# Performance work log

Hardware: AMD Instinct MI355X
Metric: run time of the kernel (lower is better)

The kernel has to match this reference:

```python
import jax, jax.numpy as jnp
import numpy as np

D_MODEL = 256
N_HEADS = 8
N_LEVELS = 4
N_POINTS = 4
D_FFN = 1024
DH = D_MODEL // N_HEADS
SPATIAL = [(100, 100), (50, 50), (25, 25), (13, 13)]  # (H_l, W_l) per level


def setup_inputs() -> dict:
    key = jax.random.key(0)
    ks = iter(jax.random.split(key, 40))
    N, Lq = 8, 900
    Lin = sum(h * w for h, w in SPATIAL)
    p = lambda shape: jax.random.normal(next(ks), shape, jnp.float32) * 0.02
    inp = {
        'idx': 0,
        'tgt': jax.random.normal(next(ks), (N, Lq, D_MODEL), jnp.float32),
        'query_pos': jax.random.normal(next(ks), (N, Lq, D_MODEL), jnp.float32),
        'reference_points_def': jax.random.uniform(next(ks), (N, Lq, N_LEVELS, 2), jnp.float32),
        'src': jax.random.normal(next(ks), (N, Lin, D_MODEL), jnp.float32),
        'src_spatial_shapes': jnp.array(SPATIAL, jnp.int32),
        'level_start_index': jnp.array(np.cumsum([0] + [h * w for h, w in SPATIAL])[:-1], jnp.int32),
        'src_padding_mask': jnp.zeros((N, Lin), bool),
        # self-attn params
        'wq': p((D_MODEL, D_MODEL)), 'bq': jnp.zeros((D_MODEL,)),
        'wk': p((D_MODEL, D_MODEL)), 'bk': jnp.zeros((D_MODEL,)),
        'wv': p((D_MODEL, D_MODEL)), 'bv': jnp.zeros((D_MODEL,)),
        'wo': p((D_MODEL, D_MODEL)), 'bo': jnp.zeros((D_MODEL,)),
        # MSDeformAttn params
        'w_val': p((D_MODEL, D_MODEL)), 'b_val': jnp.zeros((D_MODEL,)),
        'w_off': p((D_MODEL, N_HEADS * N_LEVELS * N_POINTS * 2)), 'b_off': p((N_HEADS * N_LEVELS * N_POINTS * 2,)),
        'w_att': p((D_MODEL, N_HEADS * N_LEVELS * N_POINTS)), 'b_att': jnp.zeros((N_HEADS * N_LEVELS * N_POINTS,)),
        'w_out': p((D_MODEL, D_MODEL)), 'b_out': jnp.zeros((D_MODEL,)),
        # layer norms
        'ln1_g': jnp.ones((D_MODEL,)), 'ln1_b': jnp.zeros((D_MODEL,)),
        'ln2_g': jnp.ones((D_MODEL,)), 'ln2_b': jnp.zeros((D_MODEL,)),
        'ln3_g': jnp.ones((D_MODEL,)), 'ln3_b': jnp.zeros((D_MODEL,)),
        # FFN
        'w1': p((D_MODEL, D_FFN)), 'b1': jnp.zeros((D_FFN,)),
        'w2': p((D_FFN, D_MODEL)), 'b2': jnp.zeros((D_MODEL,)),
    }
    return inp


def _ln(x, g, b):
    m = x.mean(-1, keepdims=True)
    v = jnp.var(x, axis=-1, keepdims=True)
    return (x - m) / jnp.sqrt(v + 1e-5) * g + b


def _mha(q, k, v, wq, bq, wk, bk, wv, bv, wo, bo):
    N, Lq, _ = q.shape
    split = lambda x: x.reshape(N, -1, N_HEADS, DH).transpose(0, 2, 1, 3)  # (N,H,L,dh)
    qh = split(q @ wq + bq) * (1.0 / np.sqrt(DH))
    kh = split(k @ wk + bk)
    vh = split(v @ wv + bv)
    attn = jax.nn.softmax(jnp.einsum('bhqd,bhkd->bhqk', qh, kh), axis=-1)
    o = jnp.einsum('bhqk,bhkd->bhqd', attn, vh).transpose(0, 2, 1, 3).reshape(N, Lq, D_MODEL)
    return o @ wo + bo


def _bilinear(vflat, Hl, Wl, loc):
    # vflat: (N, H, Hl*Wl, dh); loc: (N, Lq, H, P, 2) normalized (x, y) in [0,1]
    N, Lq, _, P, _ = loc.shape
    x = loc[..., 0] * Wl - 0.5  # align_corners=False pixel coords
    y = loc[..., 1] * Hl - 0.5
    x0 = jnp.floor(x); y0 = jnp.floor(y)
    fx = (x - x0).transpose(0, 2, 1, 3).reshape(N, N_HEADS, Lq * P, 1)
    fy = (y - y0).transpose(0, 2, 1, 3).reshape(N, N_HEADS, Lq * P, 1)
    x0i = x0.astype(jnp.int32); y0i = y0.astype(jnp.int32)

    def gather(xi, yi):
        valid = ((xi >= 0) & (xi < Wl) & (yi >= 0) & (yi < Hl)).astype(vflat.dtype)
        idx = jnp.clip(yi, 0, Hl - 1) * Wl + jnp.clip(xi, 0, Wl - 1)
        idx = idx.transpose(0, 2, 1, 3).reshape(N, N_HEADS, Lq * P)
        g = jnp.take_along_axis(vflat, idx[..., None], axis=2)  # (N,H,Lq*P,dh)
        return g * valid.transpose(0, 2, 1, 3).reshape(N, N_HEADS, Lq * P, 1)

    v = (gather(x0i, y0i) * (1 - fx) * (1 - fy)
         + gather(x0i + 1, y0i) * fx * (1 - fy)
         + gather(x0i, y0i + 1) * (1 - fx) * fy
         + gather(x0i + 1, y0i + 1) * fx * fy)
    return v.reshape(N, N_HEADS, Lq, P, DH)


def _msdeform(query, ref, src, ss, pad_mask, w_val, b_val, w_off, b_off, w_att, b_att, w_out, b_out):
    N, Lq, _ = query.shape
    value = src @ w_val + b_val
    value = jnp.where(pad_mask[..., None], 0.0, value)  # masked_fill on padded memory
    off = (query @ w_off + b_off).reshape(N, Lq, N_HEADS, N_LEVELS, N_POINTS, 2)
    att = jax.nn.softmax((query @ w_att + b_att).reshape(N, Lq, N_HEADS, N_LEVELS * N_POINTS), axis=-1)
    att = att.reshape(N, Lq, N_HEADS, N_LEVELS, N_POINTS)
    normalizer = jnp.array([[w, h] for h, w in ss], jnp.float32)  # (L, 2) as (W_l, H_l)
    loc = ref[:, :, None, :, None, :] + off / normalizer[None, None, None, :, None, :]
    out = jnp.zeros((N, N_HEADS, Lq, DH), value.dtype)
    start = 0
    for l, (Hl, Wl) in enumerate(ss):
        vflat = value[:, start:start + Hl * Wl].reshape(N, Hl * Wl, N_HEADS, DH).transpose(0, 2, 1, 3)
        samp = _bilinear(vflat, Hl, Wl, loc[:, :, :, l])  # (N,H,Lq,P,dh)
        w_l = att[:, :, :, l].transpose(0, 2, 1, 3)  # (N,H,Lq,P)
        out = out + (samp * w_l[..., None]).sum(3)
        start += Hl * Wl
    out = out.transpose(0, 2, 1, 3).reshape(N, Lq, D_MODEL)
    return out @ w_out + b_out, loc


def reference(idx, tgt, query_pos, reference_points_def, src, src_spatial_shapes, level_start_index,
              src_padding_mask, wq, bq, wk, bk, wv, bv, wo, bo,
              w_val, b_val, w_off, b_off, w_att, b_att, w_out, b_out,
              ln1_g, ln1_b, ln2_g, ln2_b, ln3_g, ln3_b, w1, b1, w2, b2):
    ss = [tuple(int(v) for v in row) for row in np.asarray(src_spatial_shapes)]
    # self-attention (is_contrastive=False path)
    q = tgt + query_pos
    tgt2 = _mha(q, q, tgt, wq, bq, wk, bk, wv, bv, wo, bo)
    tgt = _ln(tgt + tgt2, ln2_g, ln2_b)
    # multiscale deformable cross-attention
    tgt2, _ = _msdeform(tgt + query_pos, reference_points_def, src, ss, src_padding_mask,
                        w_val, b_val, w_off, b_off, w_att, b_att, w_out, b_out)
    tgt = _ln(tgt + tgt2, ln1_g, ln1_b)
    # FFN
    tgt2 = jax.nn.relu(tgt @ w1 + b1) @ w2 + b2
    tgt = _ln(tgt + tgt2, ln3_g, ln3_b)
    return tgt
```

## Files before the change

### kernel.cpp

```cpp
#include <hip/hip_runtime.h>
#include <math.h>

#define NB 8
#define LQ 900
#define DM 256
#define NH 8
#define DH 32
#define NL 4
#define NP 4
#define DFFN 1024
#define LIN 13294
#define NVAL (NB*LIN)
#define MROW (NB*LQ)

typedef __attribute__((ext_vector_type(8))) short bf16x8;
typedef __attribute__((ext_vector_type(4))) float f32x4;

__device__ __forceinline__ unsigned short f2bf(float x) {
  unsigned u = __float_as_uint(x);
  u += 0x7FFFu + ((u >> 16) & 1u);
  return (unsigned short)(u >> 16);
}

__global__ __launch_bounds__(256) void add_kernel(const float* __restrict__ a,
                                                  const float* __restrict__ b,
                                                  float* __restrict__ c, int n4) {
  int i = blockIdx.x * 256 + threadIdx.x;
  if (i < n4) {
    float4 x = ((const float4*)a)[i];
    float4 y = ((const float4*)b)[i];
    ((float4*)c)[i] = make_float4(x.x + y.x, x.y + y.y, x.z + y.z, x.w + y.w);
  }
}

__global__ __launch_bounds__(256) void pack_w(const float* __restrict__ Win,
                                              unsigned short* __restrict__ Wp) {
  const int idx = blockIdx.x * 256 + threadIdx.x;
  const int e = idx & 7;
  const int cs = (idx >> 3) & 3;
  const int n = (idx >> 5) & 255;
  const int kt = idx >> 13;
  const int c = cs ^ ((n >> 1) & 3);
  const int k = kt * 32 + c * 8 + e;
  Wp[idx] = f2bf(Win[(size_t)k * 256 + n]);
}

__global__ __launch_bounds__(256) void value_gemm2(const float* __restrict__ A,
                                                   const unsigned short* __restrict__ Wp,
                                                   const float* __restrict__ bias,
                                                   unsigned short* __restrict__ C,
                                                   int M) {
  __shared__ char lds[17408];
  short* As = (short*)lds;
  short* Bs = (short*)(lds + 4096);
  const int tid = threadIdx.x;
  const int lane = tid & 63, w = tid >> 6;
  const int wr = w >> 1, wc = w & 1;
  const int l15 = lane & 15, lc = lane >> 4;
  const int nwg = gridDim.x;
  const int qq = nwg >> 3, rr = nwg & 7;
  const int xcd = blockIdx.x & 7, pos = blockIdx.x >> 3;
  const int wgid = (xcd < rr ? xcd * (qq + 1) : rr * (qq + 1) + (xcd - rr) * qq) + pos;
  const int m0 = (wgid >> 1) * 64, n0 = (wgid & 1) * 128;
  const int ar = tid >> 2, ac = tid & 3;
  f32x4 acc[2][4] = {};
  for (int kt = 0; kt < 8; kt++) {
    const int arow = min(m0 + ar, M - 1);
    const float* ap = A + (size_t)arow * 256 + kt * 32 + ac * 8;
    const float4 a0 = ((const float4*)ap)[0], a1 = ((const float4*)ap)[1];
    const unsigned short* bp = Wp + ((size_t)(kt * 256 + n0)) * 32 + tid * 16;
    const uint4 b0 = ((const uint4*)bp)[0], b1 = ((const uint4*)bp)[1];
    __syncthreads();
    {
      bf16x8 av;
      av[0] = (short)f2bf(a0.x); av[1] = (short)f2bf(a0.y);
      av[2] = (short)f2bf(a0.z); av[3] = (short)f2bf(a0.w);
      av[4] = (short)f2bf(a1.x); av[5] = (short)f2bf(a1.y);
      av[6] = (short)f2bf(a1.z); av[7] = (short)f2bf(a1.w);
      *(bf16x8*)&As[ar * 32 + ((ac ^ ((ar >> 1) & 3)) << 3)] = av;
      *(uint4*)&Bs[tid * 16] = b0;
      *(uint4*)&Bs[tid * 16 + 8] = b1;
    }
    __syncthreads();
    bf16x8 af[2], bq[4];
#pragma unroll
    for (int i = 0; i < 2; i++) {
      const int row = wr * 32 + i * 16 + l15;
      af[i] = *(const bf16x8*)&As[row * 32 + ((lc ^ ((row >> 1) & 3)) << 3)];
    }
#pragma unroll
    for (int q = 0; q < 4; q++) {
      const int col = wc * 64 + q * 16 + l15;
      bq[q] = *(const bf16x8*)&Bs[col * 32 + ((lc ^ ((col >> 1) & 3)) << 3)];
    }
#pragma unroll
    for (int i = 0; i < 2; i++)
#pragma unroll
      for (int q = 0; q < 4; q++)
        acc[i][q] = __builtin_amdgcn_mfma_f32_16x16x32_bf16(af[i], bq[q], acc[i][q], 0, 0, 0);
  }
  __syncthreads();
  short* strip = (short*)lds + w * 2176;
  float bv[4];
#pragma unroll
  for (int q = 0; q < 4; q++) bv[q] = bias[n0 + wc * 64 + q * 16 + l15];
#pragma unroll
  for (int i = 0; i < 2; i++)
#pragma unroll
    for (int q = 0; q < 4; q++)
#pragma unroll
      for (int r = 0; r < 4; r++)
        strip[(i * 16 + lc * 4 + r) * 68 + q * 16 + l15] = (short)f2bf(acc[i][q][r] + bv[q]);
  __syncthreads();
#pragma unroll
  for (int p = 0; p < 4; p++) {
    const int row = p * 8 + (lane >> 3), c8 = lane & 7;
    const bf16x8 v = *(const bf16x8*)&strip[row * 68 + c8 * 8];
    const int grow = m0 + wr * 32 + row;
    if (grow < M)
      *(bf16x8*)(C + (size_t)grow * 256 + n0 + wc * 64 + c8 * 8) = v;
  }
}

#define LDSW 40
__global__ __launch_bounds__(256) void gemm_bf16(const float* __restrict__ A,
                                                 const float* __restrict__ W,
                                                 const float* __restrict__ bias,
                                                 float* __restrict__ C,
                                                 int M, int Nn, int K, float scale, int relu,
                                                 int out_bf16) {
  __shared__ short As[64 * LDSW];
  __shared__ short Bs[64 * LDSW];
  const int tid = threadIdx.x;
  const int lane = tid & 63, w = tid >> 6;
  const int wr = w >> 1, wc = w & 1;
  const int m0 = blockIdx.y << 6, n0 = blockIdx.x << 6;
  const int ar = tid >> 2, ac = (tid & 3) << 3;
  const int bk = tid >> 3, bn = (tid & 7) << 3;
  const int aswz = (((ac >> 3) ^ (ar >> 3)) & 3) << 3;
  const int l15 = lane & 15, lc = lane >> 4;
  f32x4 acc[2][2] = {};
  for (int kt = 0; kt < K; kt += 32) {
    float4 a0 = make_float4(0.f, 0.f, 0.f, 0.f), a1 = a0;
    if (m0 + ar < M) {
      const float* ap = A + (size_t)(m0 + ar) * K + kt + ac;
      a0 = ((const float4*)ap)[0]; a1 = ((const float4*)ap)[1];
    }
    const float* wp = W + (size_t)(kt + bk) * Nn + n0 + bn;
    const float4 b0 = ((const float4*)wp)[0], b1 = ((const float4*)wp)[1];
    __syncthreads();
    {
      bf16x8 av;
      av[0] = (short)f2bf(a0.x); av[1] = (short)f2bf(a0.y);
      av[2] = (short)f2bf(a0.z); av[3] = (short)f2bf(a0.w);
      av[4] = (short)f2bf(a1.x); av[5] = (short)f2bf(a1.y);
      av[6] = (short)f2bf(a1.z); av[7] = (short)f2bf(a1.w);
      *(bf16x8*)&As[ar * LDSW + aswz] = av;
      unsigned short bb[8] = {f2bf(b0.x), f2bf(b0.y), f2bf(b0.z), f2bf(b0.w),
                              f2bf(b1.x), f2bf(b1.y), f2bf(b1.z), f2bf(b1.w)};
      const int bchunk = bk >> 3, bke = bk & 7;
#pragma unroll
      for (int j = 0; j < 8; j++) {
        const int n = bn + j;
        Bs[n * LDSW + (((bchunk ^ (n >> 3)) & 3) << 3) + bke] = (short)bb[j];
      }
    }
    __syncthreads();
    bf16x8 af[2], bf[2];
#pragma unroll
    for (int i = 0; i < 2; i++) {
      const int row = wr * 32 + i * 16 + l15;
      af[i] = *(const bf16x8*)&As[row * LDSW + (((lc ^ (row >> 3)) & 3) << 3)];
      const int col = wc * 32 + i * 16 + l15;
      bf[i] = *(const bf16x8*)&Bs[col * LDSW + (((lc ^ (col >> 3)) & 3) << 3)];
    }
#pragma unroll
    for (int i = 0; i < 2; i++)
#pragma unroll
      for (int j = 0; j < 2; j++)
        acc[i][j] = __builtin_amdgcn_mfma_f32_16x16x32_bf16(af[i], bf[j], acc[i][j], 0, 0, 0);
  }
#pragma unroll
  for (int i = 0; i < 2; i++) {
    const int row0 = m0 + wr * 32 + i * 16 + lc * 4;
#pragma unroll
    for (int j = 0; j < 2; j++) {
      const int col = n0 + wc * 32 + j * 16 + l15;
      const float bv = bias[col];
#pragma unroll
      for (int r = 0; r < 4; r++) {
        const int row = row0 + r;
        if (row < M) {
          float v = (acc[i][j][r] + bv) * scale;
          if (relu) v = fmaxf(v, 0.f);
          if (out_bf16)
            ((unsigned short*)C)[(size_t)row * Nn + col] = f2bf(v);
          else
            C[(size_t)row * Nn + col] = v;
        }
      }
    }
  }
}

__global__ __launch_bounds__(256) void attn_mfma(const float* __restrict__ Qg,
                                                 const float* __restrict__ Kg,
                                                 const float* __restrict__ Vg,
                                                 float* __restrict__ O) {
  __shared__ short Ks[2048];
  __shared__ short Vt[2048];
  __shared__ short Pl[4096];
  const int tid = threadIdx.x;
  const int lane = tid & 63, w = tid >> 6;
  const int l15 = lane & 15, lc = lane >> 4;
  const int h = blockIdx.y, b = blockIdx.z;
  const int q0 = blockIdx.x * 64;
  char* KsB = (char*)Ks; char* VtB = (char*)Vt; char* PlB = (char*)Pl + w * 2048;

  bf16x8 qa;
  {
    const int qrow = min(q0 + w * 16 + l15, LQ - 1);
    const float* qp = Qg + ((size_t)(b * LQ + qrow)) * DM + h * DH + lc * 8;
    const float4 qx = ((const float4*)qp)[0], qy = ((const float4*)qp)[1];
    qa[0] = (short)f2bf(qx.x); qa[1] = (short)f2bf(qx.y);
    qa[2] = (short)f2bf(qx.z); qa[3] = (short)f2bf(qx.w);
    qa[4] = (short)f2bf(qy.x); qa[5] = (short)f2bf(qy.y);
    qa[6] = (short)f2bf(qy.z); qa[7] = (short)f2bf(qy.w);
  }
  f32x4 o0 = {0.f, 0.f, 0.f, 0.f}, o1 = {0.f, 0.f, 0.f, 0.f};
  float mrow[4], lrow[4];
#pragma unroll
  for (int r = 0; r < 4; r++) { mrow[r] = -1e30f; lrow[r] = 0.f; }
  const int skey = tid >> 2, sq = tid & 3;

  for (int kt = 0; kt < LQ; kt += 64) {
    const int kr = min(kt + skey, LQ - 1);
    const float* kp = Kg + ((size_t)(b * LQ + kr)) * DM + h * DH + sq * 8;
    const float* vp = Vg + ((size_t)(b * LQ + kr)) * DM + h * DH + sq * 8;
    const float4 k0 = ((const float4*)kp)[0], k1 = ((const float4*)kp)[1];
    const float4 v0 = ((const float4*)vp)[0], v1 = ((const float4*)vp)[1];
    __syncthreads();
    {
      bf16x8 kb;
      kb[0] = (short)f2bf(k0.x); kb[1] = (short)f2bf(k0.y);
      kb[2] = (short)f2bf(k0.z); kb[3] = (short)f2bf(k0.w);
      kb[4] = (short)f2bf(k1.x); kb[5] = (short)f2bf(k1.y);
      kb[6] = (short)f2bf(k1.z); kb[7] = (short)f2bf(k1.w);
      *(bf16x8*)(KsB + ((skey * 64 + sq * 16) ^ ((skey & 7) << 4))) = kb;
      unsigned short vv[8] = {f2bf(v0.x), f2bf(v0.y), f2bf(v0.z), f2bf(v0.w),
                              f2bf(v1.x), f2bf(v1.y), f2bf(v1.z), f2bf(v1.w)};
#pragma unroll
      for (int j = 0; j < 8; j++) {
        const int dh = sq * 8 + j;
        const int qz = ((dh & 7) ^ (((dh >> 3) & 3) << 1)) << 4;
        *(short*)(VtB + ((dh * 128 + skey * 2) ^ qz)) = (short)vv[j];
      }
    }
    __syncthreads();
    f32x4 s[4];
#pragma unroll
    for (int cb = 0; cb < 4; cb++) {
      const int key = cb * 16 + l15;
      const bf16x8 kf = *(const bf16x8*)(KsB + ((key * 64 + lc * 16) ^ ((key & 7) << 4)));
      const f32x4 z = {0.f, 0.f, 0.f, 0.f};
      s[cb] = __builtin_amdgcn_mfma_f32_16x16x32_bf16(qa, kf, z, 0, 0, 0);
    }
#pragma unroll
    for (int cb = 0; cb < 4; cb++)
      if (kt + cb * 16 + l15 >= LQ) {
        s[cb][0] = -1e30f; s[cb][1] = -1e30f; s[cb][2] = -1e30f; s[cb][3] = -1e30f;
      }
    float tm[4], fs[4], ps[4];
#pragma unroll
    for (int r = 0; r < 4; r++)
      tm[r] = fmaxf(fmaxf(s[0][r], s[1][r]), fmaxf(s[2][r], s[3][r]));
#pragma unroll
    for (int msk = 1; msk <= 8; msk <<= 1)
#pragma unroll
      for (int r = 0; r < 4; r++) tm[r] = fmaxf(tm[r], __shfl_xor(tm[r], msk));
#pragma unroll
    for (int r = 0; r < 4; r++) {
      const float nm = fmaxf(mrow[r], tm[r]);
      fs[r] = __expf(mrow[r] - nm);
      mrow[r] = nm;
    }
#pragma unroll
    for (int cb = 0; cb < 4; cb++)
#pragma unroll
      for (int r = 0; r < 4; r++) s[cb][r] = __expf(s[cb][r] - mrow[r]);
#pragma unroll
    for (int r = 0; r < 4; r++) ps[r] = (s[0][r] + s[1][r]) + (s[2][r] + s[3][r]);
#pragma unroll
    for (int msk = 1; msk <= 8; msk <<= 1)
#pragma unroll
      for (int r = 0; r < 4; r++) ps[r] += __shfl_xor(ps[r], msk);
#pragma unroll
    for (int r = 0; r < 4; r++) {
      lrow[r] = lrow[r] * fs[r] + ps[r];
      o0[r] *= fs[r]; o1[r] *= fs[r];
    }
#pragma unroll
    for (int cb = 0; cb < 4; cb++)
#pragma unroll
      for (int r = 0; r < 4; r++) {
        const int row = lc * 4 + r, col = cb * 16 + l15;
        *(short*)(PlB + ((row * 128 + col * 2) ^ ((row & 7) << 4))) = (short)f2bf(s[cb][r]);
      }
#pragma unroll
    for (int ks2 = 0; ks2 < 2; ks2++) {
      const int koff2 = (ks2 * 32 + lc * 8) * 2;
      const bf16x8 pa = *(const bf16x8*)(PlB + ((l15 * 128 + koff2) ^ ((l15 & 7) << 4)));
      {
        const int dh = l15;
        const int qz = ((dh & 7) ^ (((dh >> 3) & 3) << 1)) << 4;
        const bf16x8 vf = *(const bf16x8*)(VtB + ((dh * 128 + koff2) ^ qz));
        o0 = __builtin_amdgcn_mfma_f32_16x16x32_bf16(pa, vf, o0, 0, 0, 0);
      }
      {
        const int dh = 16 + l15;
        const int qz = ((dh & 7) ^ (((dh >> 3) & 3) << 1)) << 4;
        const bf16x8 vf = *(const bf16x8*)(VtB + ((dh * 128 + koff2) ^ qz));
        o1 = __builtin_amdgcn_mfma_f32_16x16x32_bf16(pa, vf, o1, 0, 0, 0);
      }
    }
  }
#pragma unroll
  for (int r = 0; r < 4; r++) {
    const int qrow = q0 + w * 16 + lc * 4 + r;
    if (qrow < LQ) {
      const float inv = 1.f / lrow[r];
      float* op = O + ((size_t)(b * LQ + qrow)) * DM + h * DH;
      op[l15] = o0[r] * inv;
      op[16 + l15] = o1[r] * inv;
    }
  }
}

__global__ __launch_bounds__(256) void sample_kernel(const unsigned short* __restrict__ value,
                                                     const float* __restrict__ ref,
                                                     const float* __restrict__ off,
                                                     const float* __restrict__ att,
                                                     float* __restrict__ out) {
  const int t = blockIdx.x * 256 + threadIdx.x;
  const int d8 = t & 3;
  const int h = (t >> 2) & 7;
  const int qb = t >> 5;
  const int b = qb / LQ;
  const int HLs[4] = {100, 50, 25, 13};
  const int STs[4] = {0, 10000, 12500, 13125};
  const float* rp = ref + (size_t)qb * (NL * 2);
  const float* op = off + (size_t)qb * DM + h * (NL * NP * 2);
  const float* ap = att + (size_t)qb * (NH * NL * NP) + h * (NL * NP);
  const unsigned short* vb = value + (size_t)b * LIN * DM + h * DH + d8 * 8;

  float aw[16];
#pragma unroll
  for (int i = 0; i < 4; i++) {
    const float4 a4 = ((const float4*)ap)[i];
    aw[4 * i] = a4.x; aw[4 * i + 1] = a4.y; aw[4 * i + 2] = a4.z; aw[4 * i + 3] = a4.w;
  }
  float am = aw[0];
#pragma unroll
  for (int i = 1; i < 16; i++) am = fmaxf(am, aw[i]);
  float asum = 0.f;
#pragma unroll
  for (int i = 0; i < 16; i++) { aw[i] = __expf(aw[i] - am); asum += aw[i]; }
  const float ainv = 1.f / asum;

  float acc[8] = {};
#pragma unroll
  for (int l = 0; l < NL; l++) {
    const int Hl = HLs[l], Wl = HLs[l], st = STs[l];
    const float rx = rp[l * 2], ry = rp[l * 2 + 1];
#pragma unroll
    for (int p = 0; p < NP; p++) {
      const float2 o2 = ((const float2*)op)[l * NP + p];
      const float a = aw[l * NP + p] * ainv;
      const float locx = rx + o2.x / (float)Wl;
      const float locy = ry + o2.y / (float)Hl;
      const float x = locx * (float)Wl - 0.5f;
      const float y = locy * (float)Hl - 0.5f;
      const float xf = floorf(x), yf = floorf(y);
      const float fx = x - xf, fy = y - yf;
      const int x0 = (int)xf, y0 = (int)yf;
      const int x1 = x0 + 1, y1 = y0 + 1;
      const float vx0 = (x0 >= 0 && x0 < Wl) ? 1.f : 0.f;
      const float vx1 = (x1 >= 0 && x1 < Wl) ? 1.f : 0.f;
      const float vy0 = (y0 >= 0 && y0 < Hl) ? 1.f : 0.f;
      const float vy1 = (y1 >= 0 && y1 < Hl) ? 1.f : 0.f;
      const int cx0 = min(max(x0, 0), Wl - 1), cx1 = min(max(x1, 0), Wl - 1);
      const int cy0 = min(max(y0, 0), Hl - 1), cy1 = min(max(y1, 0), Hl - 1);
      const float w00 = a * (1.f - fx) * (1.f - fy) * vx0 * vy0;
      const float w10 = a * fx * (1.f - fy) * vx1 * vy0;
      const float w01 = a * (1.f - fx) * fy * vx0 * vy1;
      const float w11 = a * fx * fy * vx1 * vy1;
      const unsigned short* r0 = vb + (size_t)(st + cy0 * Wl) * DM;
      const unsigned short* r1 = vb + (size_t)(st + cy1 * Wl) * DM;
      const uint4 g00 = *(const uint4*)(r0 + (size_t)cx0 * DM);
      const uint4 g10 = *(const uint4*)(r0 + (size_t)cx1 * DM);
      const uint4 g01 = *(const uint4*)(r1 + (size_t)cx0 * DM);
      const uint4 g11 = *(const uint4*)(r1 + (size_t)cx1 * DM);
      const unsigned u00[4] = {g00.x, g00.y, g00.z, g00.w};
      const unsigned u10[4] = {g10.x, g10.y, g10.z, g10.w};
      const unsigned u01[4] = {g01.x, g01.y, g01.z, g01.w};
      const unsigned u11[4] = {g11.x, g11.y, g11.z, g11.w};
#pragma unroll
      for (int i = 0; i < 4; i++) {
        acc[2 * i]     += w00 * __uint_as_float(u00[i] << 16) + w10 * __uint_as_float(u10[i] << 16)
                        + w01 * __uint_as_float(u01[i] << 16) + w11 * __uint_as_float(u11[i] << 16);
        acc[2 * i + 1] += w00 * __uint_as_float(u00[i] & 0xFFFF0000u) + w10 * __uint_as_float(u10[i] & 0xFFFF0000u)
                        + w01 * __uint_as_float(u01[i] & 0xFFFF0000u) + w11 * __uint_as_float(u11[i] & 0xFFFF0000u);
      }
    }
  }
  float* o = out + (size_t)t * 8;
  *(float4*)o = make_float4(acc[0], acc[1], acc[2], acc[3]);
  *(float4*)(o + 4) = make_float4(acc[4], acc[5], acc[6], acc[7]);
}

__global__ __launch_bounds__(64) void ln_kernel(const float* __restrict__ A,
                                                const float* __restrict__ R,
                                                const float* __restrict__ g,
                                                const float* __restrict__ be,
                                                float* __restrict__ out) {
  const int row = blockIdx.x, t = threadIdx.x;
  const float4 va = ((const float4*)(A + (size_t)row * DM))[t];
  const float4 vr = ((const float4*)(R + (size_t)row * DM))[t];
  const float x0 = va.x + vr.x, x1 = va.y + vr.y, x2 = va.z + vr.z, x3 = va.w + vr.w;
  float s = x0 + x1 + x2 + x3;
  float ss = x0 * x0 + x1 * x1 + x2 * x2 + x3 * x3;
#pragma unroll
  for (int o = 1; o < 64; o <<= 1) { s += __shfl_xor(s, o); ss += __shfl_xor(ss, o); }
  const float mean = s * (1.f / DM);
  const float var = ss * (1.f / DM) - mean * mean;
  const float rstd = rsqrtf(var + 1e-5f);
  const float4 vg = ((const float4*)g)[t];
  const float4 vb = ((const float4*)be)[t];
  float4 o4;
  o4.x = (x0 - mean) * rstd * vg.x + vb.x;
  o4.y = (x1 - mean) * rstd * vg.y + vb.y;
  o4.z = (x2 - mean) * rstd * vg.z + vb.z;
  o4.w = (x3 - mean) * rstd * vg.w + vb.w;
  ((float4*)(out + (size_t)row * DM))[t] = o4;
}

extern "C" void kernel_launch(void* const* d_in, const int* in_sizes, int n_in,
                              void* d_out, int out_size, void* d_ws, size_t ws_size,
                              hipStream_t stream) {
  const float* tgt  = (const float*)d_in[1];
  const float* qpos = (const float*)d_in[2];
  const float* ref  = (const float*)d_in[3];
  const float* src  = (const float*)d_in[4];
  const float* wq = (const float*)d_in[8];  const float* bq = (const float*)d_in[9];
  const float* wk = (const float*)d_in[10]; const float* bk = (const float*)d_in[11];
  const float* wv = (const float*)d_in[12]; const float* bv = (const float*)d_in[13];
  const float* wo = (const float*)d_in[14]; const float* bo = (const float*)d_in[15];
  const float* w_val = (const float*)d_in[16]; const float* b_val = (const float*)d_in[17];
  const float* w_off = (const float*)d_in[18]; const float* b_off = (const float*)d_in[19];
  const float* w_att = (const float*)d_in[20]; const float* b_att = (const float*)d_in[21];
  const float* w_out = (const float*)d_in[22]; const float* b_out = (const float*)d_in[23];
  const float* ln1g = (const float*)d_in[24]; const float* ln1b = (const float*)d_in[25];
  const float* ln2g = (const float*)d_in[26]; const float* ln2b = (const float*)d_in[27];
  const float* ln3g = (const float*)d_in[28]; const float* ln3b = (const float*)d_in[29];
  const float* w1 = (const float*)d_in[30]; const float* b1 = (const float*)d_in[31];
  const float* w2 = (const float*)d_in[32]; const float* b2 = (const float*)d_in[33];

  const size_t S = (size_t)MROW * DM;
  const size_t VAL_F = (size_t)NVAL * DM;
  float* ws = (float*)d_ws;
  float* value = ws;
  unsigned short* wp = (unsigned short*)(ws + VAL_F / 2);
  float* B0   = ws + VAL_F;
  float* qin  = B0 + 0 * S;
  float* Qb   = B0 + 1 * S;
  float* Kb   = B0 + 2 * S;
  float* Vb   = B0 + 3 * S;
  float* Ob   = B0 + 4 * S;
  float* tmp  = B0 + 5 * S;
  float* x1   = B0 + 0 * S;
  float* q2   = B0 + 1 * S;
  float* offb = B0 + 2 * S;
  float* attb = B0 + 3 * S;
  float* samp = B0 + 4 * S;
  float* x2   = B0 + 6 * S;
  float* hffn = B0 + 1 * S;

  const float qscale = 0.17677669529663687f;
  const int n4 = (int)(S / 4);
  const dim3 blk(256);
  const dim3 gAdd((n4 + 255) / 256);
  const dim3 gQ(DM / 64, (MROW + 63) / 64);
  const dim3 gAtt(2, (MROW + 63) / 64);
  const dim3 gF1(DFFN / 64, (MROW + 63) / 64);
  const int gVal2 = 2 * ((NVAL + 63) / 64);

  add_kernel<<<gAdd, blk, 0, stream>>>(tgt, qpos, qin, n4);
  gemm_bf16<<<gQ, blk, 0, stream>>>(qin, wq, bq, Qb, MROW, DM, DM, qscale, 0, 0);
  gemm_bf16<<<gQ, blk, 0, stream>>>(qin, wk, bk, Kb, MROW, DM, DM, 1.f, 0, 0);
  gemm_bf16<<<gQ, blk, 0, stream>>>(tgt, wv, bv, Vb, MROW, DM, DM, 1.f, 0, 0);
  attn_mfma<<<dim3((LQ + 63) / 64, NH, NB), blk, 0, stream>>>(Qb, Kb, Vb, Ob);
  gemm_bf16<<<gQ, blk, 0, stream>>>(Ob, wo, bo, tmp, MROW, DM, DM, 1.f, 0, 0);
  ln_kernel<<<dim3(MROW), dim3(64), 0, stream>>>(tmp, tgt, ln2g, ln2b, x1);

  pack_w<<<dim3(256), blk, 0, stream>>>(w_val, wp);
  value_gemm2<<<dim3(gVal2), blk, 0, stream>>>(src, wp, b_val, (unsigned short*)value, NVAL);
  add_kernel<<<gAdd, blk, 0, stream>>>(x1, qpos, q2, n4);
  gemm_bf16<<<gQ, blk, 0, stream>>>(q2, w_off, b_off, offb, MROW, DM, DM, 1.f, 0, 0);
  gemm_bf16<<<gAtt, blk, 0, stream>>>(q2, w_att, b_att, attb, MROW, NH * NL * NP, DM, 1.f, 0, 0);
  sample_kernel<<<dim3((MROW * NH * 4) / 256), blk, 0, stream>>>(
      (const unsigned short*)value, ref, offb, attb, samp);
  gemm_bf16<<<gQ, blk, 0, stream>>>(samp, w_out, b_out, tmp, MROW, DM, DM, 1.f, 0, 0);
  ln_kernel<<<dim3(MROW), dim3(64), 0, stream>>>(tmp, x1, ln1g, ln1b, x2);

  gemm_bf16<<<gF1, blk, 0, stream>>>(x2, w1, b1, hffn, MROW, DFFN, DM, 1.f, 1, 0);
  gemm_bf16<<<gQ, blk, 0, stream>>>(hffn, w2, b2, tmp, MROW, DM, DFFN, 1.f, 0, 0);
  ln_kernel<<<dim3(MROW), dim3(64), 0, stream>>>(tmp, x2, ln3g, ln3b, (float*)d_out);
}
```

Before: 279.7 us.

## Fuse residual adds into GEMMs, batch QKV and offset/attn GEMMs, use bf16 intermediates

Removes the two elementwise add kernels by folding the query_pos add into the A-operand load of the GEMMs. The Q/K/V projections become one launch indexed by blockIdx.z, and so do the offset and attention-weight projections. Q/K/V and the FFN hidden activations are now stored as bf16, which halves intermediate traffic and drops the conversions in attention and the second FFN GEMM. The cost is extra branching in a shared GEMM body, and out-of-range A rows are now clamped instead of zero-filled.

```diff
diff --git a/kernel.cpp b/kernel.cpp
--- a/kernel.cpp
+++ b/kernel.cpp
@@ -20,17 +20,6 @@
   unsigned u = __float_as_uint(x);
   u += 0x7FFFu + ((u >> 16) & 1u);
   return (unsigned short)(u >> 16);
-}
-
-__global__ __launch_bounds__(256) void add_kernel(const float* __restrict__ a,
-                                                  const float* __restrict__ b,
-                                                  float* __restrict__ c, int n4) {
-  int i = blockIdx.x * 256 + threadIdx.x;
-  if (i < n4) {
-    float4 x = ((const float4*)a)[i];
-    float4 y = ((const float4*)b)[i];
-    ((float4*)c)[i] = make_float4(x.x + y.x, x.y + y.y, x.z + y.z, x.w + y.w);
-  }
 }
 
 __global__ __launch_bounds__(256) void pack_w(const float* __restrict__ Win,
@@ -123,38 +112,43 @@
 }
 
 #define LDSW 40
-__global__ __launch_bounds__(256) void gemm_bf16(const float* __restrict__ A,
-                                                 const float* __restrict__ W,
-                                                 const float* __restrict__ bias,
-                                                 float* __restrict__ C,
-                                                 int M, int Nn, int K, float scale, int relu,
-                                                 int out_bf16) {
-  __shared__ short As[64 * LDSW];
-  __shared__ short Bs[64 * LDSW];
+__device__ __forceinline__ void gemm_body(const void* Aptr, const float* A2,
+                                          const float* __restrict__ W,
+                                          const float* __restrict__ bias, void* Cptr,
+                                          int M, int Nn, int K, float scale, int relu,
+                                          int a_bf16, int out_bf16, int m0, int n0,
+                                          short* As, short* Bs) {
   const int tid = threadIdx.x;
   const int lane = tid & 63, w = tid >> 6;
   const int wr = w >> 1, wc = w & 1;
-  const int m0 = blockIdx.y << 6, n0 = blockIdx.x << 6;
   const int ar = tid >> 2, ac = (tid & 3) << 3;
   const int bk = tid >> 3, bn = (tid & 7) << 3;
   const int aswz = (((ac >> 3) ^ (ar >> 3)) & 3) << 3;
   const int l15 = lane & 15, lc = lane >> 4;
+  const int arow = min(m0 + ar, M - 1);
   f32x4 acc[2][2] = {};
   for (int kt = 0; kt < K; kt += 32) {
-    float4 a0 = make_float4(0.f, 0.f, 0.f, 0.f), a1 = a0;
-    if (m0 + ar < M) {
-      const float* ap = A + (size_t)(m0 + ar) * K + kt + ac;
-      a0 = ((const float4*)ap)[0]; a1 = ((const float4*)ap)[1];
+    bf16x8 av;
+    if (a_bf16) {
+      av = *(const bf16x8*)((const unsigned short*)Aptr + (size_t)arow * K + kt + ac);
+    } else {
+      const float* ap = (const float*)Aptr + (size_t)arow * K + kt + ac;
+      float4 a0 = ((const float4*)ap)[0], a1 = ((const float4*)ap)[1];
+      if (A2) {
+        const float* a2p = A2 + (size_t)arow * K + kt + ac;
+        const float4 c0 = ((const float4*)a2p)[0], c1 = ((const float4*)a2p)[1];
+        a0.x += c0.x; a0.y += c0.y; a0.z += c0.z; a0.w += c0.w;
+        a1.x += c1.x; a1.y += c1.y; a1.z += c1.z; a1.w += c1.w;
+      }
+      av[0] = (short)f2bf(a0.x); av[1] = (short)f2bf(a0.y);
+      av[2] = (short)f2bf(a0.z); av[3] = (short)f2bf(a0.w);
+      av[4] = (short)f2bf(a1.x); av[5] = (short)f2bf(a1.y);
+      av[6] = (short)f2bf(a1.z); av[7] = (short)f2bf(a1.w);
     }
     const float* wp = W + (size_t)(kt + bk) * Nn + n0 + bn;
     const float4 b0 = ((const float4*)wp)[0], b1 = ((const float4*)wp)[1];
     __syncthreads();
     {
-      bf16x8 av;
-      av[0] = (short)f2bf(a0.x); av[1] = (short)f2bf(a0.y);
-      av[2] = (short)f2bf(a0.z); av[3] = (short)f2bf(a0.w);
-      av[4] = (short)f2bf(a1.x); av[5] = (short)f2bf(a1.y);
-      av[6] = (short)f2bf(a1.z); av[7] = (short)f2bf(a1.w);
       *(bf16x8*)&As[ar * LDSW + aswz] = av;
       unsigned short bb[8] = {f2bf(b0.x), f2bf(b0.y), f2bf(b0.z), f2bf(b0.w),
                               f2bf(b1.x), f2bf(b1.y), f2bf(b1.z), f2bf(b1.w)};
@@ -194,18 +188,62 @@
           float v = (acc[i][j][r] + bv) * scale;
           if (relu) v = fmaxf(v, 0.f);
           if (out_bf16)
-            ((unsigned short*)C)[(size_t)row * Nn + col] = f2bf(v);
+            ((unsigned short*)Cptr)[(size_t)row * Nn + col] = f2bf(v);
           else
-            C[(size_t)row * Nn + col] = v;
+            ((float*)Cptr)[(size_t)row * Nn + col] = v;
         }
       }
     }
   }
 }
 
-__global__ __launch_bounds__(256) void attn_mfma(const float* __restrict__ Qg,
-                                                 const float* __restrict__ Kg,
-                                                 const float* __restrict__ Vg,
+__global__ __launch_bounds__(256) void gemm_qkv(const float* __restrict__ tgt,
+                                                const float* __restrict__ qpos,
+                                                const float* __restrict__ wq, const float* __restrict__ bq_,
+                                                const float* __restrict__ wk, const float* __restrict__ bk_,
+                                                const float* __restrict__ wv, const float* __restrict__ bv_,
+                                                unsigned short* Qb, unsigned short* Kb, unsigned short* Vb,
+                                                float qscale) {
+  __shared__ short As[64 * LDSW];
+  __shared__ short Bs[64 * LDSW];
+  const int z = blockIdx.z;
+  const float* W = (z == 0) ? wq : (z == 1) ? wk : wv;
+  const float* bias = (z == 0) ? bq_ : (z == 1) ? bk_ : bv_;
+  unsigned short* C = (z == 0) ? Qb : (z == 1) ? Kb : Vb;
+  const float* A2 = (z == 2) ? nullptr : qpos;
+  gemm_body(tgt, A2, W, bias, C, MROW, DM, DM, (z == 0) ? qscale : 1.f, 0, 0, 1,
+            blockIdx.y * 64, blockIdx.x * 64, As, Bs);
+}
+
+__global__ __launch_bounds__(256) void gemm_offatt(const float* __restrict__ x1,
+                                                   const float* __restrict__ qpos,
+                                                   const float* __restrict__ w_off, const float* __restrict__ b_off,
+                                                   const float* __restrict__ w_att, const float* __restrict__ b_att,
+                                                   float* offb, float* attb) {
+  const int z = blockIdx.z;
+  if (z == 1 && blockIdx.x >= 2) return;
+  __shared__ short As[64 * LDSW];
+  __shared__ short Bs[64 * LDSW];
+  const float* W = z ? w_att : w_off;
+  const float* bias = z ? b_att : b_off;
+  float* C = z ? attb : offb;
+  const int Nn = z ? 128 : 256;
+  gemm_body(x1, qpos, W, bias, C, MROW, Nn, DM, 1.f, 0, 0, 0,
+            blockIdx.y * 64, blockIdx.x * 64, As, Bs);
+}
+
+__global__ __launch_bounds__(256) void gemm_fused(const void* A, const float* W, const float* bias,
+                                                  void* C, int M, int Nn, int K, float scale,
+                                                  int relu, int a_bf16, int out_bf16) {
+  __shared__ short As[64 * LDSW];
+  __shared__ short Bs[64 * LDSW];
+  gemm_body(A, nullptr, W, bias, C, M, Nn, K, scale, relu, a_bf16, out_bf16,
+            blockIdx.y * 64, blockIdx.x * 64, As, Bs);
+}
+
+__global__ __launch_bounds__(256) void attn_mfma(const unsigned short* __restrict__ Qg,
+                                                 const unsigned short* __restrict__ Kg,
+                                                 const unsigned short* __restrict__ Vg,
                                                  float* __restrict__ O) {
   __shared__ short Ks[2048];
   __shared__ short Vt[2048];
@@ -220,12 +258,7 @@
   bf16x8 qa;
   {
     const int qrow = min(q0 + w * 16 + l15, LQ - 1);
-    const float* qp = Qg + ((size_t)(b * LQ + qrow)) * DM + h * DH + lc * 8;
-    const float4 qx = ((const float4*)qp)[0], qy = ((const float4*)qp)[1];
-    qa[0] = (short)f2bf(qx.x); qa[1] = (short)f2bf(qx.y);
-    qa[2] = (short)f2bf(qx.z); qa[3] = (short)f2bf(qx.w);
-    qa[4] = (short)f2bf(qy.x); qa[5] = (short)f2bf(qy.y);
-    qa[6] = (short)f2bf(qy.z); qa[7] = (short)f2bf(qy.w);
+    qa = *(const bf16x8*)(Qg + ((size_t)(b * LQ + qrow)) * DM + h * DH + lc * 8);
   }
   f32x4 o0 = {0.f, 0.f, 0.f, 0.f}, o1 = {0.f, 0.f, 0.f, 0.f};
   float mrow[4], lrow[4];
@@ -235,20 +268,11 @@
 
   for (int kt = 0; kt < LQ; kt += 64) {
     const int kr = min(kt + skey, LQ - 1);
-    const float* kp = Kg + ((size_t)(b * LQ + kr)) * DM + h * DH + sq * 8;
-    const float* vp = Vg + ((size_t)(b * LQ + kr)) * DM + h * DH + sq * 8;
-    const float4 k0 = ((const float4*)kp)[0], k1 = ((const float4*)kp)[1];
-    const float4 v0 = ((const float4*)vp)[0], v1 = ((const float4*)vp)[1];
+    const bf16x8 kb = *(const bf16x8*)(Kg + ((size_t)(b * LQ + kr)) * DM + h * DH + sq * 8);
+    const bf16x8 vv = *(const bf16x8*)(Vg + ((size_t)(b * LQ + kr)) * DM + h * DH + sq * 8);
     __syncthreads();
     {
-      bf16x8 kb;
-      kb[0] = (short)f2bf(k0.x); kb[1] = (short)f2bf(k0.y);
-      kb[2] = (short)f2bf(k0.z); kb[3] = (short)f2bf(k0.w);
-      kb[4] = (short)f2bf(k1.x); kb[5] = (short)f2bf(k1.y);
-      kb[6] = (short)f2bf(k1.z); kb[7] = (short)f2bf(k1.w);
       *(bf16x8*)(KsB + ((skey * 64 + sq * 16) ^ ((skey & 7) << 4))) = kb;
-      unsigned short vv[8] = {f2bf(v0.x), f2bf(v0.y), f2bf(v0.z), f2bf(v0.w),
-                              f2bf(v1.x), f2bf(v1.y), f2bf(v1.z), f2bf(v1.w)};
 #pragma unroll
       for (int j = 0; j < 8; j++) {
         const int dh = sq * 8 + j;
@@ -471,48 +495,40 @@
   float* value = ws;
   unsigned short* wp = (unsigned short*)(ws + VAL_F / 2);
   float* B0   = ws + VAL_F;
-  float* qin  = B0 + 0 * S;
-  float* Qb   = B0 + 1 * S;
-  float* Kb   = B0 + 2 * S;
-  float* Vb   = B0 + 3 * S;
+  unsigned short* Qb = (unsigned short*)(B0 + 1 * S);
+  unsigned short* Kb = (unsigned short*)(B0 + 2 * S);
+  unsigned short* Vb = (unsigned short*)(B0 + 3 * S);
   float* Ob   = B0 + 4 * S;
   float* tmp  = B0 + 5 * S;
   float* x1   = B0 + 0 * S;
-  float* q2   = B0 + 1 * S;
   float* offb = B0 + 2 * S;
   float* attb = B0 + 3 * S;
   float* samp = B0 + 4 * S;
   float* x2   = B0 + 6 * S;
-  float* hffn = B0 + 1 * S;
+  unsigned short* hffn = (unsigned short*)(B0 + 1 * S);
 
   const float qscale = 0.17677669529663687f;
-  const int n4 = (int)(S / 4);
   const dim3 blk(256);
-  const dim3 gAdd((n4 + 255) / 256);
   const dim3 gQ(DM / 64, (MROW + 63) / 64);
-  const dim3 gAtt(2, (MROW + 63) / 64);
-  const dim3 gF1(DFFN / 64, (MROW + 63) / 64);
   const int gVal2 = 2 * ((NVAL + 63) / 64);
 
-  add_kernel<<<gAdd, blk, 0, stream>>>(tgt, qpos, qin, n4);
-  gemm_bf16<<<gQ, blk, 0, stream>>>(qin, wq, bq, Qb, MROW, DM, DM, qscale, 0, 0);
-  gemm_bf16<<<gQ, blk, 0, stream>>>(qin, wk, bk, Kb, MROW, DM, DM, 1.f, 0, 0);
-  gemm_bf16<<<gQ, blk, 0, stream>>>(tgt, wv, bv, Vb, MROW, DM, DM, 1.f, 0, 0);
+  gemm_qkv<<<dim3(4, 113, 3), blk, 0, stream>>>(tgt, qpos, wq, bq, wk, bk, wv, bv,
+                                                Qb, Kb, Vb, qscale);
   attn_mfma<<<dim3((LQ + 63) / 64, NH, NB), blk, 0, stream>>>(Qb, Kb, Vb, Ob);
-  gemm_bf16<<<gQ, blk, 0, stream>>>(Ob, wo, bo, tmp, MROW, DM, DM, 1.f, 0, 0);
+  gemm_fused<<<gQ, blk, 0, stream>>>(Ob, wo, bo, tmp, MROW, DM, DM, 1.f, 0, 0, 0);
   ln_kernel<<<dim3(MROW), dim3(64), 0, stream>>>(tmp, tgt, ln2g, ln2b, x1);
 
   pack_w<<<dim3(256), blk, 0, stream>>>(w_val, wp);
   value_gemm2<<<dim3(gVal2), blk, 0, stream>>>(src, wp, b_val, (unsigned short*)value, NVAL);
-  add_kernel<<<gAdd, blk, 0, stream>>>(x1, qpos, q2, n4);
-  gemm_bf16<<<gQ, blk, 0, stream>>>(q2, w_off, b_off, offb, MROW, DM, DM, 1.f, 0, 0);
-  gemm_bf16<<<gAtt, blk, 0, stream>>>(q2, w_att, b_att, attb, MROW, NH * NL * NP, DM, 1.f, 0, 0);
+  gemm_offatt<<<dim3(4, 113, 2), blk, 0, stream>>>(x1, qpos, w_off, b_off, w_att, b_att,
+                                                   offb, attb);
   sample_kernel<<<dim3((MROW * NH * 4) / 256), blk, 0, stream>>>(
       (const unsigned short*)value, ref, offb, attb, samp);
-  gemm_bf16<<<gQ, blk, 0, stream>>>(samp, w_out, b_out, tmp, MROW, DM, DM, 1.f, 0, 0);
+  gemm_fused<<<gQ, blk, 0, stream>>>(samp, w_out, b_out, tmp, MROW, DM, DM, 1.f, 0, 0, 0);
   ln_kernel<<<dim3(MROW), dim3(64), 0, stream>>>(tmp, x1, ln1g, ln1b, x2);
 
-  gemm_bf16<<<gF1, blk, 0, stream>>>(x2, w1, b1, hffn, MROW, DFFN, DM, 1.f, 1, 0);
-  gemm_bf16<<<gQ, blk, 0, stream>>>(hffn, w2, b2, tmp, MROW, DM, DFFN, 1.f, 0, 0);
+  gemm_fused<<<dim3(DFFN / 64, 113), blk, 0, stream>>>(x2, w1, b1, hffn, MROW, DFFN, DM,
+                                                       1.f, 1, 0, 1);
+  gemm_fused<<<gQ, blk, 0, stream>>>(hffn, w2, b2, tmp, MROW, DM, DFFN, 1.f, 0, 1, 0);
   ln_kernel<<<dim3(MROW), dim3(64), 0, stream>>>(tmp, x2, ln3g, ln3b, (float*)d_out);
 }
```

Result: faster. 257.2 us (-8.1%).
